# Kernel optimization log

Measured on AMD Instinct MI355X. Metric: run time of the kernel, lower is better.

The kernel has to match this reference:

```python
import jax, jax.numpy as jnp
import numpy as np

B, N = 32, 4096
SA1 = (512, 0.2, 32)   # npoint, radius, nsample
SA2 = (128, 0.4, 64)
MLP1 = [3, 64, 64, 128]
MLP2 = [131, 128, 128, 256]   # 128 feats + 3 relative xyz
MLP3 = [259, 256, 512, 1024]  # 256 feats + 3 xyz (group_all)


def _mk_mlp(key, dims, prefix, d):
    for i in range(len(dims) - 1):
        key, k1 = jax.random.split(key)
        d[f"{prefix}_w{i}"] = jax.random.normal(k1, (dims[i], dims[i + 1]), jnp.float32) * (1.0 / np.sqrt(dims[i]))
        d[f"{prefix}_b{i}"] = jnp.zeros((dims[i + 1],), jnp.float32)
    return key


def setup_inputs() -> dict:
    key = jax.random.key(0)
    d = {}
    key, kx = jax.random.split(key)
    d["xyz"] = jax.random.uniform(kx, (B, N, 3), jnp.float32)  # normalized coords in [0,1)
    key = _mk_mlp(key, MLP1, "sa1", d)
    key = _mk_mlp(key, MLP2, "sa2", d)
    key = _mk_mlp(key, MLP3, "sa3", d)
    key, k1, k2 = jax.random.split(key, 3)
    d["cls_w"] = jax.random.normal(k1, (1024, 1), jnp.float32) * 0.03
    d["cls_b"] = jnp.zeros((1,), jnp.float32)
    d["reg_w"] = jax.random.normal(k2, (1024, 4), jnp.float32) * 0.03
    d["reg_b"] = jnp.zeros((4,), jnp.float32)
    return d


def fps(xyz, npoint):
    """Farthest point sampling. xyz: (B,N,3) -> idx (B,npoint) int32."""
    Bb, Nn, _ = xyz.shape

    def step(carry, _):
        dist, farthest = carry  # (B,N), (B,)
        centroid = jnp.take_along_axis(xyz, farthest[:, None, None], axis=1)  # (B,1,3)
        d = jnp.sum((xyz - centroid) ** 2, axis=-1)  # (B,N)
        dist = jnp.minimum(dist, d)
        nxt = jnp.argmax(dist, axis=-1).astype(jnp.int32)
        return (dist, nxt), farthest

    init = (jnp.full((Bb, Nn), 1e10, xyz.dtype), jnp.zeros((Bb,), jnp.int32))
    _, idx = jax.lax.scan(step, init, None, length=npoint)
    return idx.T  # (B,npoint)


def ball_query(radius, nsample, xyz, new_xyz):
    """xyz: (B,N,3), new_xyz: (B,S,3) -> idx (B,S,nsample) int32."""
    Bb, S, _ = new_xyz.shape
    Nn = xyz.shape[1]
    sqr = jnp.sum((new_xyz[:, :, None, :] - xyz[:, None, :, :]) ** 2, axis=-1)  # (B,S,N)
    idx = jnp.broadcast_to(jnp.arange(Nn, dtype=jnp.int32), (Bb, S, Nn))
    idx = jnp.where(sqr > radius * radius, Nn, idx)
    idx = jnp.sort(idx, axis=-1)[:, :, :nsample]
    first = idx[:, :, :1]
    return jnp.where(idx == Nn, first, idx)  # pad out-of-ball slots with first neighbor


def _sa(xyz, feats, npoint, radius, nsample, ws, bs):
    Bb = xyz.shape[0]
    cidx = fps(xyz, npoint)
    new_xyz = xyz[jnp.arange(Bb)[:, None], cidx]  # (B,S,3)
    gidx = ball_query(radius, nsample, xyz, new_xyz)  # (B,S,K)
    b3 = jnp.arange(Bb)[:, None, None]
    g = xyz[b3, gidx] - new_xyz[:, :, None, :]  # (B,S,K,3) relative coords
    if feats is not None:
        g = jnp.concatenate([g, feats[b3, gidx]], axis=-1)
    for w, b in zip(ws, bs):
        g = jax.nn.relu(g @ w + b)
    return new_xyz, jnp.max(g, axis=2)  # (B,S,C_out)


def _sa_all(xyz, feats, ws, bs):
    g = jnp.concatenate([xyz, feats], axis=-1)[:, None]  # (B,1,S,3+C)
    for w, b in zip(ws, bs):
        g = jax.nn.relu(g @ w + b)
    return jnp.max(g, axis=2)[:, 0]  # (B,C_out)


def reference(xyz, sa1_w0, sa1_b0, sa1_w1, sa1_b1, sa1_w2, sa1_b2,
              sa2_w0, sa2_b0, sa2_w1, sa2_b1, sa2_w2, sa2_b2,
              sa3_w0, sa3_b0, sa3_w1, sa3_b1, sa3_w2, sa3_b2,
              cls_w, cls_b, reg_w, reg_b):
    xyz1, f1 = _sa(xyz, None, SA1[0], SA1[1], SA1[2],
                   [sa1_w0, sa1_w1, sa1_w2], [sa1_b0, sa1_b1, sa1_b2])
    xyz2, f2 = _sa(xyz1, f1, SA2[0], SA2[1], SA2[2],
                   [sa2_w0, sa2_w1, sa2_w2], [sa2_b0, sa2_b1, sa2_b2])
    feat = _sa_all(xyz2, f2, [sa3_w0, sa3_w1, sa3_w2], [sa3_b0, sa3_b1, sa3_b2])  # (B,1024)
    return feat @ cls_w + cls_b, feat @ reg_w + reg_b
```

## Files before the change

kernel.cpp:

```cpp
#include <hip/hip_runtime.h>
#include <hip/hip_bf16.h>

#define DEVINL __device__ __forceinline__

typedef __attribute__((ext_vector_type(8))) short bf16x8;
typedef __attribute__((ext_vector_type(8))) unsigned short u16x8;
typedef __attribute__((ext_vector_type(4))) float f32x4;

DEVINL unsigned short f2bh(float f){
  __hip_bfloat16 h = __float2bfloat16(f);
  return __bfloat16_as_ushort(h);
}
DEVINL float bh2f(unsigned short h){ return __uint_as_float(((unsigned)h) << 16); }

DEVINL unsigned long long dpp_max_u64(unsigned long long k) {
#define DPP_STEP(ctrl)                                                        \
  {                                                                           \
    int hi = (int)(k >> 32), lo = (int)(unsigned)k;                           \
    int oh = __builtin_amdgcn_update_dpp(0, hi, ctrl, 0xF, 0xF, 1);           \
    int ol = __builtin_amdgcn_update_dpp(0, lo, ctrl, 0xF, 0xF, 1);           \
    unsigned long long ok =                                                   \
        ((unsigned long long)(unsigned)oh << 32) | (unsigned)ol;              \
    if (ok > k) k = ok;                                                       \
  }
  DPP_STEP(0x111)
  DPP_STEP(0x112)
  DPP_STEP(0x114)
  DPP_STEP(0x118)
  DPP_STEP(0x142)
  DPP_STEP(0x143)
#undef DPP_STEP
  return k;
}

template<int N, int NP, int NT>
DEVINL void fps_body(const float* __restrict__ xyz, float* __restrict__ nxyz,
                     int b, int t) {
  constexpr int PTS = N / NT;
  constexpr int NW = NT / 64;
  __shared__ float xs[N], ys[N], zs[N];
  __shared__ int farr[NP];
  __shared__ unsigned long long sk[2][(NW > 1 ? NW : 1)];
  float px[PTS], py[PTS], pz[PTS], dst[PTS];
  const float* base = xyz + (size_t)b * N * 3;
#pragma unroll
  for (int j = 0; j < PTS; ++j) {
    int i = t + j * NT;
    float x = base[i * 3 + 0], y = base[i * 3 + 1], z = base[i * 3 + 2];
    px[j] = x; py[j] = y; pz[j] = z;
    xs[i] = x; ys[i] = y; zs[i] = z;
    dst[j] = 1e10f;
  }
  if constexpr (NW > 1) __syncthreads();
  int far = 0;
  const int wv = t >> 6, ln = t & 63;
  for (int s = 0; s < NP; ++s) {
    float cx = xs[far], cy = ys[far], cz = zs[far];
    if (t == 0) farr[s] = far;
    float bv = -1.f; int bi = 0;
#pragma unroll
    for (int j = 0; j < PTS; ++j) {
      float dx = __fsub_rn(px[j], cx), dy = __fsub_rn(py[j], cy), dz = __fsub_rn(pz[j], cz);
      float d = __fadd_rn(__fadd_rn(__fmul_rn(dx, dx), __fmul_rn(dy, dy)), __fmul_rn(dz, dz));
      float nd = fminf(dst[j], d);
      dst[j] = nd;
      int i = t + j * NT;
      if (nd > bv) { bv = nd; bi = i; }
    }
    unsigned long long key =
        ((unsigned long long)__float_as_uint(bv) << 32) | (unsigned)(~bi);
    key = dpp_max_u64(key);
    if constexpr (NW == 1) {
      int rl = __builtin_amdgcn_readlane((int)(unsigned)key, 63);
      far = (int)(~(unsigned)rl);
    } else {
      const int p = s & 1;
      if (ln == 63) sk[p][wv] = key;
      __syncthreads();
      unsigned long long m = sk[p][0];
#pragma unroll
      for (int q = 1; q < NW; ++q) {
        unsigned long long qk = sk[p][q];
        if (qk > m) m = qk;
      }
      far = (int)(~(unsigned)m);
    }
  }
  if constexpr (NW > 1) __syncthreads();
  for (int s2 = t; s2 < NP; s2 += NT) {
    int fi = farr[s2];
    float* o = nxyz + ((size_t)b * NP + s2) * 3;
    o[0] = xs[fi]; o[1] = ys[fi]; o[2] = zs[fi];
  }
}

template<int N, int NS>
DEVINL void bq_body(const float* __restrict__ pts, const float* __restrict__ centers,
                    int* __restrict__ gidx, int Q, float r2, int blk, int t) {
  const int wv = t >> 6, ln = t & 63;
  const int g = blk * 4 + wv;
  const int b = g / Q, q = g % Q;
  const float* pb = pts + (size_t)b * N * 3;
  const float* c = centers + ((size_t)b * Q + q) * 3;
  const float cx = c[0], cy = c[1], cz = c[2];
  __shared__ int gbuf[4][NS];
  float nx = pb[ln * 3 + 0], ny = pb[ln * 3 + 1], nz = pb[ln * 3 + 2];
  int taken = 0;
  for (int base = 0; base < N; base += 64) {
    const float x = nx, y = ny, z = nz;
    if (base + 64 < N) {
      const float* np = pb + (size_t)(base + 64 + ln) * 3;
      nx = np[0]; ny = np[1]; nz = np[2];
    }
    int i = base + ln;
    float dx = __fsub_rn(x, cx), dy = __fsub_rn(y, cy), dz = __fsub_rn(z, cz);
    float d = __fadd_rn(__fadd_rn(__fmul_rn(dx, dx), __fmul_rn(dy, dy)), __fmul_rn(dz, dz));
    bool in = (d <= r2);
    unsigned long long mk = __ballot(in);
    int rank = __popcll(mk & ((1ull << ln) - 1ull));
    int pos = taken + rank;
    if (in && pos < NS) gbuf[wv][pos] = i;
    taken += (int)__popcll(mk);
    if (taken >= NS) break;
  }
  int total = taken < NS ? taken : NS;
  int first = gbuf[wv][0];
  int* out = gidx + ((size_t)b * Q + q) * NS;
  for (int j = ln; j < NS; j += 64) out[j] = (j < total) ? gbuf[wv][j] : first;
}

struct WPEnt { const float* W; unsigned short* hi; unsigned short* lo; int K, N, row0, beg, end; };
struct WPTab { WPEnt e[8]; };
DEVINL void wprep_body(const WPTab& tab, int idx) {
#pragma unroll
  for (int i = 0; i < 8; ++i) {
    const WPEnt& E = tab.e[i];
    if (idx >= E.beg && idx < E.end) {
      int local = idx - E.beg;
      int k = local / E.N, n = local - k * E.N;
      float v = E.W[(size_t)(E.row0 + k) * E.N + n];
      unsigned short h = f2bh(v);
      E.hi[(size_t)n * E.K + k] = h;
      E.lo[(size_t)n * E.K + k] = f2bh(v - bh2f(h));
    }
  }
}

__global__ __launch_bounds__(256) void fps1_wprep_kernel(const float* __restrict__ xyz,
                                                         float* __restrict__ nx1, WPTab tab) {
  if (blockIdx.x < 32) { fps_body<4096, 512, 256>(xyz, nx1, blockIdx.x, threadIdx.x); return; }
  wprep_body(tab, (blockIdx.x - 32) * 256 + threadIdx.x);
}

__global__ __launch_bounds__(256) void fps2_bq1_kernel(const float* __restrict__ xyz,
                                                       const float* __restrict__ nx1,
                                                       int* __restrict__ gidx1,
                                                       float* __restrict__ nx2, float r21) {
  if (blockIdx.x < 32) {
    if (threadIdx.x < 64) fps_body<512, 128, 64>(nx1, nx2, blockIdx.x, threadIdx.x);
    return;
  }
  bq_body<4096, 32>(xyz, nx1, gidx1, 512, r21, blockIdx.x - 32, threadIdx.x);
}

template<int K, int N, int CW, int AS, int WS, bool XYZC, int NTH>
DEVINL void do_layer(const unsigned short* __restrict__ Ghi, const unsigned short* __restrict__ Glo,
                     const float* __restrict__ Wxyz,
                     const float* __restrict__ A, unsigned short* __restrict__ Whi,
                     unsigned short* __restrict__ Wlo, const float* __restrict__ sxyz,
                     f32x4* acc, int t) {
  constexpr int KT = K / 32;
  constexpr int NCH = N / CW;
  constexpr int K8 = K / 8;
  constexpr int SI = (CW * K8) / NTH;
  constexpr int CT = CW / 16;
  const int l = t & 63, wv = t >> 6;

  u16x8 rh[SI], rl[SI];
#pragma unroll
  for (int s = 0; s < SI; ++s) {
    int u = t + s * NTH;
    int nn = u / K8, k8 = (u - nn * K8) * 8;
    rh[s] = *reinterpret_cast<const u16x8*>(Ghi + (size_t)nn * K + k8);
    rl[s] = *reinterpret_cast<const u16x8*>(Glo + (size_t)nn * K + k8);
  }

  bf16x8 ahi[KT], alo[KT];
  {
    const int row = wv * 16 + (l & 15);
    const float* ap = A + row * AS + (l >> 4) * 8;
#pragma unroll
    for (int kt = 0; kt < KT; ++kt) {
      float4 v0 = *reinterpret_cast<const float4*>(ap + kt * 32);
      float4 v1 = *reinterpret_cast<const float4*>(ap + kt * 32 + 4);
      float f[8] = {v0.x, v0.y, v0.z, v0.w, v1.x, v1.y, v1.z, v1.w};
      bf16x8 h, lo2;
#pragma unroll
      for (int j = 0; j < 8; ++j) {
        unsigned short hb = f2bh(f[j]);
        h[j] = (short)hb;
        lo2[j] = (short)f2bh(f[j] - bh2f(hb));
      }
      ahi[kt] = h; alo[kt] = lo2;
    }
  }
#pragma unroll
  for (int i = 0; i < N / 16; ++i) acc[i] = f32x4{0.f, 0.f, 0.f, 0.f};

#pragma unroll
  for (int c = 0; c < NCH; ++c) {
    __syncthreads();
#pragma unroll
    for (int s = 0; s < SI; ++s) {
      int u = t + s * NTH;
      int nn = u / K8, k8 = (u - nn * K8) * 8;
      *reinterpret_cast<u16x8*>(Whi + nn * WS + k8) = rh[s];
      *reinterpret_cast<u16x8*>(Wlo + nn * WS + k8) = rl[s];
    }
    if (c + 1 < NCH) {
#pragma unroll
      for (int s = 0; s < SI; ++s) {
        int u = t + s * NTH;
        int nn = u / K8, k8 = (u - nn * K8) * 8;
        rh[s] = *reinterpret_cast<const u16x8*>(Ghi + (size_t)((c + 1) * CW + nn) * K + k8);
        rl[s] = *reinterpret_cast<const u16x8*>(Glo + (size_t)((c + 1) * CW + nn) * K + k8);
      }
    }
    __syncthreads();
#pragma unroll
    for (int ct = 0; ct < CT; ++ct) {
      const unsigned short* wp = Whi + (ct * 16 + (l & 15)) * WS + (l >> 4) * 8;
      const unsigned short* wq = Wlo + (ct * 16 + (l & 15)) * WS + (l >> 4) * 8;
      f32x4 a = acc[c * CT + ct];
#pragma unroll
      for (int kt = 0; kt < KT; ++kt) {
        bf16x8 wh = *reinterpret_cast<const bf16x8*>(wp + kt * 32);
        bf16x8 wl = *reinterpret_cast<const bf16x8*>(wq + kt * 32);
        a = __builtin_amdgcn_mfma_f32_16x16x32_bf16(ahi[kt], wh, a, 0, 0, 0);
        a = __builtin_amdgcn_mfma_f32_16x16x32_bf16(alo[kt], wh, a, 0, 0, 0);
        a = __builtin_amdgcn_mfma_f32_16x16x32_bf16(ahi[kt], wl, a, 0, 0, 0);
      }
      acc[c * CT + ct] = a;
    }
  }
  if constexpr (XYZC) {
    float xr[4][3];
#pragma unroll
    for (int r = 0; r < 4; ++r) {
      int row = wv * 16 + (l >> 4) * 4 + r;
      xr[r][0] = sxyz[row * 4 + 0];
      xr[r][1] = sxyz[row * 4 + 1];
      xr[r][2] = sxyz[row * 4 + 2];
    }
#pragma unroll
    for (int gt = 0; gt < N / 16; ++gt) {
      int col = gt * 16 + (l & 15);
      float w0 = Wxyz[col], w1 = Wxyz[N + col], w2 = Wxyz[2 * N + col];
#pragma unroll
      for (int r = 0; r < 4; ++r)
        acc[gt][r] += xr[r][0] * w0 + xr[r][1] * w1 + xr[r][2] * w2;
    }
  }
}

template<int NPTS, int Q, int M, int GPB, int FD, int C1, int C2, int C3>
__global__ __launch_bounds__(512) void sa2_kernel(
    const float* __restrict__ pts, const float* __restrict__ centers,
    const int* __restrict__ gidx, const float* __restrict__ feats,
    const float* __restrict__ W0, const float* __restrict__ B0,
    const unsigned short* __restrict__ G0h, const unsigned short* __restrict__ G0l,
    const unsigned short* __restrict__ G1h, const unsigned short* __restrict__ G1l,
    const float* __restrict__ B1,
    const unsigned short* __restrict__ G2h, const unsigned short* __restrict__ G2l,
    const float* __restrict__ B2,
    float* __restrict__ fout) {
  constexpr int NTH = 512;
  constexpr int ROWS = M * GPB;
  constexpr int NWV = NTH / 64;
  static_assert(ROWS == 16 * NWV, "wave owns 16 rows");
  constexpr int MK1 = (FD > C1 ? FD : C1);
  constexpr int MAXK = (MK1 > C2 ? MK1 : C2);
  constexpr int AS = MAXK + 12;
  constexpr int WS = MAXK + 8;
  constexpr int CW = 128;
  __shared__ __align__(16) float A[ROWS * AS];
  __shared__ __align__(16) unsigned short Whi[CW * WS];
  __shared__ __align__(16) unsigned short Wlo[CW * WS];
  __shared__ float sxyz[ROWS * 4];
  __shared__ int idxs[ROWS];
  __shared__ float ctr[GPB][4];
  __shared__ float red[NWV][C3];

  const int t = threadIdx.x;
  const int blk = blockIdx.x;
  const int b = blk / (Q / GPB);
  const int q0 = (blk % (Q / GPB)) * GPB;
  const int l = t & 63, wv = t >> 6;

  if (t < GPB * 3) {
    int g = t / 3, c2 = t % 3;
    ctr[g][c2] = centers[((size_t)b * Q + q0 + g) * 3 + c2];
  }
  for (int m = t; m < ROWS; m += NTH)
    idxs[m] = gidx[((size_t)b * Q + q0 + (m / M)) * M + (m % M)];
  __syncthreads();
  const float* pb = pts + (size_t)b * NPTS * 3;
  for (int u = t; u < ROWS * 3; u += NTH) {
    int m = u / 3, cmp = u - m * 3;
    int g = m / M, i = idxs[m];
    sxyz[m * 4 + cmp] = pb[i * 3 + cmp] - ctr[g][cmp];
  }
  {
    const int m = t >> 2, co = (t & 3) * (FD / 4);
    const float* src = feats + ((size_t)b * NPTS + idxs[m]) * FD + co;
    float* dst = A + m * AS + co;
#pragma unroll
    for (int j = 0; j < FD / 4; j += 4)
      *reinterpret_cast<float4*>(dst + j) = *reinterpret_cast<const float4*>(src + j);
  }
  __syncthreads();

  f32x4 acc[C3 / 16];

  do_layer<FD, C1, CW, AS, WS, true, NTH>(G0h, G0l, W0, A, Whi, Wlo, sxyz, acc, t);
#pragma unroll
  for (int gt = 0; gt < C1 / 16; ++gt) {
    int col = gt * 16 + (l & 15);
    float bia = B0[col];
#pragma unroll
    for (int r = 0; r < 4; ++r)
      A[(wv * 16 + (l >> 4) * 4 + r) * AS + col] = fmaxf(acc[gt][r] + bia, 0.f);
  }

  do_layer<C1, C2, CW, AS, WS, false, NTH>(G1h, G1l, nullptr, A, Whi, Wlo, sxyz, acc, t);
#pragma unroll
  for (int gt = 0; gt < C2 / 16; ++gt) {
    int col = gt * 16 + (l & 15);
    float bia = B1[col];
#pragma unroll
    for (int r = 0; r < 4; ++r)
      A[(wv * 16 + (l >> 4) * 4 + r) * AS + col] = fmaxf(acc[gt][r] + bia, 0.f);
  }

  do_layer<C2, C3, CW, AS, WS, false, NTH>(G2h, G2l, nullptr, A, Whi, Wlo, sxyz, acc, t);
#pragma unroll
  for (int gt = 0; gt < C3 / 16; ++gt) {
    int col = gt * 16 + (l & 15);
    float v = fmaxf(fmaxf(acc[gt][0], acc[gt][1]), fmaxf(acc[gt][2], acc[gt][3]));
    v = fmaxf(v, __shfl_xor(v, 16, 64));
    v = fmaxf(v, __shfl_xor(v, 32, 64));
    if (l < 16) red[wv][col] = v + B2[col];
  }
  __syncthreads();
  constexpr int WPG = NWV / GPB;
  for (int u = t; u < GPB * C3; u += NTH) {
    int g = u / C3, c2 = u - g * C3;
    float v = red[g * WPG][c2];
#pragma unroll
    for (int w = 1; w < WPG; ++w) v = fmaxf(v, red[g * WPG + w][c2]);
    fout[((size_t)b * Q + q0 + g) * C3 + c2] = fmaxf(v, 0.f);
  }
}

template<int NPTS, int Q, int M, int GPB, int TPB>
DEVINL void sa1_body(const float* __restrict__ pts, const float* __restrict__ centers,
                     const int* __restrict__ gidx,
                     const float* __restrict__ W0, const float* __restrict__ B0,
                     const unsigned short* __restrict__ G1h, const unsigned short* __restrict__ G1l,
                     const float* __restrict__ B1,
                     const unsigned short* __restrict__ G2h, const unsigned short* __restrict__ G2l,
                     const float* __restrict__ B2,
                     float* __restrict__ fout, int sblk, int t) {
  static_assert(M * GPB == 64, "");
  constexpr int C1 = 64, C2 = 64, C3 = 128;
  constexpr int AS = 76;
  constexpr int WS = 72;
  constexpr int NC = C2 + C3;
  __shared__ __align__(16) float A[64 * AS];
  __shared__ __align__(16) unsigned short Wh[NC * WS];
  __shared__ __align__(16) unsigned short Wl[NC * WS];
  __shared__ float sxyz[64 * 4];
  __shared__ int idxs[64];
  __shared__ float ctr[GPB][4];
  __shared__ float red[4][C3];

  const int l = t & 63, wv = t >> 6;

  for (int u = t; u < NC * 8; u += 256) {
    int col = u >> 3, k8 = (u & 7) * 8;
    const unsigned short* sh = (col < C2) ? G1h + (size_t)col * 64 + k8
                                          : G2h + (size_t)(col - C2) * 64 + k8;
    const unsigned short* sl = (col < C2) ? G1l + (size_t)col * 64 + k8
                                          : G2l + (size_t)(col - C2) * 64 + k8;
    *reinterpret_cast<u16x8*>(Wh + col * WS + k8) = *reinterpret_cast<const u16x8*>(sh);
    *reinterpret_cast<u16x8*>(Wl + col * WS + k8) = *reinterpret_cast<const u16x8*>(sl);
  }

  for (int it = 0; it < TPB; ++it) {
    const int blk = sblk * TPB + it;
    const int b = blk / (Q / GPB);
    const int q0 = (blk % (Q / GPB)) * GPB;

    if (t < GPB * 3) {
      int g = t / 3, c2 = t % 3;
      ctr[g][c2] = centers[((size_t)b * Q + q0 + g) * 3 + c2];
    }
    for (int m = t; m < 64; m += 256)
      idxs[m] = gidx[((size_t)b * Q + q0 + (m / M)) * M + (m % M)];
    __syncthreads();
    const float* pb = pts + (size_t)b * NPTS * 3;
    for (int u = t; u < 64 * 3; u += 256) {
      int m = u / 3, cmp = u - m * 3;
      int g = m / M, i = idxs[m];
      sxyz[m * 4 + cmp] = pb[i * 3 + cmp] - ctr[g][cmp];
    }
    __syncthreads();

    for (int u = t; u < 64 * C1; u += 256) {
      int m = u / C1, c2 = u - m * C1;
      float v = B0[c2] + sxyz[m * 4 + 0] * W0[0 * C1 + c2]
                       + sxyz[m * 4 + 1] * W0[1 * C1 + c2]
                       + sxyz[m * 4 + 2] * W0[2 * C1 + c2];
      A[m * AS + c2] = fmaxf(v, 0.f);
    }
    __syncthreads();

    f32x4 acc[8];
    {
      bf16x8 ah[2], al[2];
      const float* ap = A + (wv * 16 + (l & 15)) * AS + (l >> 4) * 8;
#pragma unroll
      for (int kt = 0; kt < 2; ++kt) {
        float4 v0 = *reinterpret_cast<const float4*>(ap + kt * 32);
        float4 v1 = *reinterpret_cast<const float4*>(ap + kt * 32 + 4);
        float f[8] = {v0.x, v0.y, v0.z, v0.w, v1.x, v1.y, v1.z, v1.w};
        bf16x8 h, lo2;
#pragma unroll
        for (int j = 0; j < 8; ++j) {
          unsigned short hb = f2bh(f[j]);
          h[j] = (short)hb;
          lo2[j] = (short)f2bh(f[j] - bh2f(hb));
        }
        ah[kt] = h; al[kt] = lo2;
      }
#pragma unroll
      for (int i = 0; i < 4; ++i) acc[i] = f32x4{0.f, 0.f, 0.f, 0.f};
#pragma unroll
      for (int ct = 0; ct < 4; ++ct) {
        const unsigned short* wp = Wh + (ct * 16 + (l & 15)) * WS + (l >> 4) * 8;
        const unsigned short* wq = Wl + (ct * 16 + (l & 15)) * WS + (l >> 4) * 8;
        f32x4 a = acc[ct];
#pragma unroll
        for (int kt = 0; kt < 2; ++kt) {
          bf16x8 wh = *reinterpret_cast<const bf16x8*>(wp + kt * 32);
          bf16x8 wl = *reinterpret_cast<const bf16x8*>(wq + kt * 32);
          a = __builtin_amdgcn_mfma_f32_16x16x32_bf16(ah[kt], wh, a, 0, 0, 0);
          a = __builtin_amdgcn_mfma_f32_16x16x32_bf16(al[kt], wh, a, 0, 0, 0);
          a = __builtin_amdgcn_mfma_f32_16x16x32_bf16(ah[kt], wl, a, 0, 0, 0);
        }
        acc[ct] = a;
      }
#pragma unroll
      for (int gt = 0; gt < 4; ++gt) {
        int col = gt * 16 + (l & 15);
        float bia = B1[col];
#pragma unroll
        for (int r = 0; r < 4; ++r)
          A[(wv * 16 + (l >> 4) * 4 + r) * AS + col] = fmaxf(acc[gt][r] + bia, 0.f);
      }
    }

    {
      bf16x8 ah[2], al[2];
      const float* ap = A + (wv * 16 + (l & 15)) * AS + (l >> 4) * 8;
#pragma unroll
      for (int kt = 0; kt < 2; ++kt) {
        float4 v0 = *reinterpret_cast<const float4*>(ap + kt * 32);
        float4 v1 = *reinterpret_cast<const float4*>(ap + kt * 32 + 4);
        float f[8] = {v0.x, v0.y, v0.z, v0.w, v1.x, v1.y, v1.z, v1.w};
        bf16x8 h, lo2;
#pragma unroll
        for (int j = 0; j < 8; ++j) {
          unsigned short hb = f2bh(f[j]);
          h[j] = (short)hb;
          lo2[j] = (short)f2bh(f[j] - bh2f(hb));
        }
        ah[kt] = h; al[kt] = lo2;
      }
#pragma unroll
      for (int i = 0; i < 8; ++i) acc[i] = f32x4{0.f, 0.f, 0.f, 0.f};
#pragma unroll
      for (int gt = 0; gt < 8; ++gt) {
        const unsigned short* wp = Wh + (C2 + gt * 16 + (l & 15)) * WS + (l >> 4) * 8;
        const unsigned short* wq = Wl + (C2 + gt * 16 + (l & 15)) * WS + (l >> 4) * 8;
        f32x4 a = acc[gt];
#pragma unroll
        for (int kt = 0; kt < 2; ++kt) {
          bf16x8 wh = *reinterpret_cast<const bf16x8*>(wp + kt * 32);
          bf16x8 wl = *reinterpret_cast<const bf16x8*>(wq + kt * 32);
          a = __builtin_amdgcn_mfma_f32_16x16x32_bf16(ah[kt], wh, a, 0, 0, 0);
          a = __builtin_amdgcn_mfma_f32_16x16x32_bf16(al[kt], wh, a, 0, 0, 0);
          a = __builtin_amdgcn_mfma_f32_16x16x32_bf16(ah[kt], wl, a, 0, 0, 0);
        }
        acc[gt] = a;
      }
#pragma unroll
      for (int gt = 0; gt < 8; ++gt) {
        int col = gt * 16 + (l & 15);
        float v = fmaxf(fmaxf(acc[gt][0], acc[gt][1]), fmaxf(acc[gt][2], acc[gt][3]));
        v = fmaxf(v, __shfl_xor(v, 16, 64));
        v = fmaxf(v, __shfl_xor(v, 32, 64));
        if (l < 16) red[wv][col] = v + B2[col];
      }
    }
    __syncthreads();
    constexpr int WPG = 4 / GPB;
    for (int u = t; u < GPB * C3; u += 256) {
      int g = u / C3, c2 = u - g * C3;
      float v = red[g * WPG][c2];
#pragma unroll
      for (int w = 1; w < WPG; ++w) v = fmaxf(v, red[g * WPG + w][c2]);
      fout[((size_t)b * Q + q0 + g) * C3 + c2] = fmaxf(v, 0.f);
    }
    __syncthreads();
  }
}

__global__ __launch_bounds__(256) void bq2_sa1_kernel(
    const float* __restrict__ xyz, const float* __restrict__ nx1,
    const float* __restrict__ nx2, int* __restrict__ gidx2, float r22,
    const int* __restrict__ gidx1,
    const float* __restrict__ s1w0, const float* __restrict__ s1b0,
    const unsigned short* __restrict__ g11h, const unsigned short* __restrict__ g11l,
    const float* __restrict__ s1b1,
    const unsigned short* __restrict__ g12h, const unsigned short* __restrict__ g12l,
    const float* __restrict__ s1b2, float* __restrict__ f1) {
  if (blockIdx.x < 1024) {
    bq_body<512, 64>(nx1, nx2, gidx2, 128, r22, blockIdx.x, threadIdx.x);
    return;
  }
  sa1_body<4096, 512, 32, 2, 8>(xyz, nx1, gidx1, s1w0, s1b0, g11h, g11l, s1b1,
                                g12h, g12l, s1b2, f1, blockIdx.x - 1024, threadIdx.x);
}

constexpr int AS3 = 532;
DEVINL void sa3_frags(const float* __restrict__ A, int l, int KT, bf16x8* ahi, bf16x8* alo) {
  const float* ap = A + (l & 15) * AS3 + (l >> 4) * 8;
  for (int kt = 0; kt < KT; ++kt) {
    float4 v0 = *reinterpret_cast<const float4*>(ap + kt * 32);
    float4 v1 = *reinterpret_cast<const float4*>(ap + kt * 32 + 4);
    float f[8] = {v0.x, v0.y, v0.z, v0.w, v1.x, v1.y, v1.z, v1.w};
    bf16x8 h, lo2;
#pragma unroll
    for (int j = 0; j < 8; ++j) {
      unsigned short hb = f2bh(f[j]);
      h[j] = (short)hb;
      lo2[j] = (short)f2bh(f[j] - bh2f(hb));
    }
    ahi[kt] = h; alo[kt] = lo2;
  }
}

template<int CT, int K>
DEVINL void sa3_mmN(const unsigned short* __restrict__ Gh, const unsigned short* __restrict__ Gl,
                    int ncol0, int l, const bf16x8* ahi, const bf16x8* alo, f32x4* acc4) {
  constexpr int KT = K / 32;
#pragma unroll
  for (int ct = 0; ct < CT; ++ct) {
    const unsigned short* hp = Gh + (size_t)(ncol0 + ct * 16 + (l & 15)) * K + (l >> 4) * 8;
    const unsigned short* lp = Gl + (size_t)(ncol0 + ct * 16 + (l & 15)) * K + (l >> 4) * 8;
    f32x4 a = acc4[ct];
#pragma unroll
    for (int kt = 0; kt < KT; ++kt) {
      bf16x8 wh = *reinterpret_cast<const bf16x8*>(hp + kt * 32);
      bf16x8 wl = *reinterpret_cast<const bf16x8*>(lp + kt * 32);
      a = __builtin_amdgcn_mfma_f32_16x16x32_bf16(ahi[kt], wh, a, 0, 0, 0);
      a = __builtin_amdgcn_mfma_f32_16x16x32_bf16(alo[kt], wh, a, 0, 0, 0);
      a = __builtin_amdgcn_mfma_f32_16x16x32_bf16(ahi[kt], wl, a, 0, 0, 0);
    }
    acc4[ct] = a;
  }
}

__global__ __launch_bounds__(512) void sa3f_kernel(
    const float* __restrict__ nx2, const float* __restrict__ f2,
    const float* __restrict__ W0full,
    const unsigned short* __restrict__ G0h, const unsigned short* __restrict__ G0l,
    const float* __restrict__ B0,
    const unsigned short* __restrict__ G1h, const unsigned short* __restrict__ G1l,
    const float* __restrict__ B1,
    const unsigned short* __restrict__ G2h, const unsigned short* __restrict__ G2l,
    const float* __restrict__ B2,
    float* __restrict__ partial) {
  __shared__ __align__(16) float A[16 * AS3];
  __shared__ float sxyz[16][4];
  const int t = threadIdx.x, l = t & 63, w = t >> 6;
  const int b = blockIdx.x >> 3, rb = blockIdx.x & 7;
  const int row0 = rb * 16;
  {
    int r = t >> 5, cc = (t & 31) * 8;
    const float* src = f2 + ((size_t)b * 128 + row0 + r) * 256 + cc;
    float* dstp = A + r * AS3 + cc;
#pragma unroll
    for (int j = 0; j < 8; j += 4)
      *reinterpret_cast<float4*>(dstp + j) = *reinterpret_cast<const float4*>(src + j);
    if (t < 16) {
      const float* s = nx2 + ((size_t)b * 128 + row0 + t) * 3;
      sxyz[t][0] = s[0]; sxyz[t][1] = s[1]; sxyz[t][2] = s[2];
    }
  }
  __syncthreads();

  {
    bf16x8 ah[8], al[8];
    sa3_frags(A, l, 8, ah, al);
    __syncthreads();
    f32x4 acc[2];
#pragma unroll
    for (int i = 0; i < 2; ++i) acc[i] = f32x4{0.f, 0.f, 0.f, 0.f};
    sa3_mmN<2, 256>(G0h, G0l, w * 32, l, ah, al, acc);
    float xr[4][3];
#pragma unroll
    for (int r = 0; r < 4; ++r) {
      int row = (l >> 4) * 4 + r;
      xr[r][0] = sxyz[row][0]; xr[r][1] = sxyz[row][1]; xr[r][2] = sxyz[row][2];
    }
#pragma unroll
    for (int ct = 0; ct < 2; ++ct) {
      int col = w * 32 + ct * 16 + (l & 15);
      float w0 = W0full[col], w1 = W0full[256 + col], w2 = W0full[512 + col];
      float bia = B0[col];
#pragma unroll
      for (int r = 0; r < 4; ++r) {
        int row = (l >> 4) * 4 + r;
        float v = acc[ct][r] + xr[r][0] * w0 + xr[r][1] * w1 + xr[r][2] * w2 + bia;
        A[row * AS3 + col] = fmaxf(v, 0.f);
      }
    }
    __syncthreads();
  }

  {
    bf16x8 ah[8], al[8];
    sa3_frags(A, l, 8, ah, al);
    __syncthreads();
    f32x4 acc[4];
#pragma unroll
    for (int i = 0; i < 4; ++i) acc[i] = f32x4{0.f, 0.f, 0.f, 0.f};
    sa3_mmN<4, 256>(G1h, G1l, w * 64, l, ah, al, acc);
#pragma unroll
    for (int cc = 0; cc < 4; ++cc) {
      int col = w * 64 + cc * 16 + (l & 15);
      float bia = B1[col];
#pragma unroll
      for (int r = 0; r < 4; ++r) {
        int row = (l >> 4) * 4 + r;
        A[row * AS3 + col] = fmaxf(acc[cc][r] + bia, 0.f);
      }
    }
    __syncthreads();
  }

  {
    bf16x8 ah[16], al[16];
    sa3_frags(A, l, 16, ah, al);
    float* pout = partial + ((size_t)(b * 8 + rb)) * 1024;
#pragma unroll
    for (int sub = 0; sub < 2; ++sub) {
      f32x4 acc[4];
#pragma unroll
      for (int i = 0; i < 4; ++i) acc[i] = f32x4{0.f, 0.f, 0.f, 0.f};
      sa3_mmN<4, 512>(G2h, G2l, w * 128 + sub * 64, l, ah, al, acc);
#pragma unroll
      for (int ct = 0; ct < 4; ++ct) {
        int col = w * 128 + sub * 64 + ct * 16 + (l & 15);
        float v = fmaxf(fmaxf(acc[ct][0], acc[ct][1]), fmaxf(acc[ct][2], acc[ct][3]));
        v = fmaxf(v, __shfl_xor(v, 16, 64));
        v = fmaxf(v, __shfl_xor(v, 32, 64));
        if (l < 16) pout[col] = v + B2[col];
      }
    }
  }
}

__global__ __launch_bounds__(256) void heads_kernel(const float* __restrict__ partial,
                                                    const float* __restrict__ cw,
                                                    const float* __restrict__ cb,
                                                    const float* __restrict__ rw,
                                                    const float* __restrict__ rb,
                                                    float* __restrict__ out) {
  const int b = blockIdx.x, t = threadIdx.x;
  const float* pb = partial + (size_t)b * 8 * 1024;
  float a0 = 0, a1 = 0, a2 = 0, a3 = 0, a4 = 0;
  for (int k = t; k < 1024; k += 256) {
    float m = pb[k];
#pragma unroll
    for (int p = 1; p < 8; ++p) m = fmaxf(m, pb[p * 1024 + k]);
    float f = fmaxf(m, 0.f);
    a0 += f * cw[k];
    const float* r = rw + (size_t)k * 4;
    a1 += f * r[0]; a2 += f * r[1]; a3 += f * r[2]; a4 += f * r[3];
  }
#pragma unroll
  for (int m = 32; m >= 1; m >>= 1) {
    a0 += __shfl_xor(a0, m, 64); a1 += __shfl_xor(a1, m, 64);
    a2 += __shfl_xor(a2, m, 64); a3 += __shfl_xor(a3, m, 64);
    a4 += __shfl_xor(a4, m, 64);
  }
  __shared__ float red[4][5];
  const int wv = t >> 6, ln = t & 63;
  if (ln == 0) { red[wv][0] = a0; red[wv][1] = a1; red[wv][2] = a2; red[wv][3] = a3; red[wv][4] = a4; }
  __syncthreads();
  if (t == 0) {
    float s0 = red[0][0] + red[1][0] + red[2][0] + red[3][0];
    float s1 = red[0][1] + red[1][1] + red[2][1] + red[3][1];
    float s2 = red[0][2] + red[1][2] + red[2][2] + red[3][2];
    float s3 = red[0][3] + red[1][3] + red[2][3] + red[3][3];
    float s4 = red[0][4] + red[1][4] + red[2][4] + red[3][4];
    out[b] = s0 + cb[0];
    out[32 + b * 4 + 0] = s1 + rb[0];
    out[32 + b * 4 + 1] = s2 + rb[1];
    out[32 + b * 4 + 2] = s3 + rb[2];
    out[32 + b * 4 + 3] = s4 + rb[3];
  }
}

extern "C" void kernel_launch(void* const* d_in, const int* in_sizes, int n_in,
                              void* d_out, int out_size, void* d_ws, size_t ws_size,
                              hipStream_t stream) {
  (void)in_sizes; (void)n_in; (void)out_size; (void)ws_size;
  const float* xyz  = (const float*)d_in[0];
  const float* s1w0 = (const float*)d_in[1];  const float* s1b0 = (const float*)d_in[2];
  const float* s1w1 = (const float*)d_in[3];  const float* s1b1 = (const float*)d_in[4];
  const float* s1w2 = (const float*)d_in[5];  const float* s1b2 = (const float*)d_in[6];
  const float* s2w0 = (const float*)d_in[7];  const float* s2b0 = (const float*)d_in[8];
  const float* s2w1 = (const float*)d_in[9];  const float* s2b1 = (const float*)d_in[10];
  const float* s2w2 = (const float*)d_in[11]; const float* s2b2 = (const float*)d_in[12];
  const float* s3w0 = (const float*)d_in[13]; const float* s3b0 = (const float*)d_in[14];
  const float* s3w1 = (const float*)d_in[15]; const float* s3b1 = (const float*)d_in[16];
  const float* s3w2 = (const float*)d_in[17]; const float* s3b2 = (const float*)d_in[18];
  const float* clsw = (const float*)d_in[19]; const float* clsb = (const float*)d_in[20];
  const float* regw = (const float*)d_in[21]; const float* regb = (const float*)d_in[22];

  char* ws = (char*)d_ws;
  float* nx1   = (float*)(ws + 0);
  int*   gidx1 = (int*)  (ws + 196608);
  float* f1    = (float*)(ws + 2293760);
  float* nx2   = (float*)(ws + 10682368);
  int*   gidx2 = (int*)  (ws + 10731520);
  float* f2    = (float*)(ws + 11780096);

  unsigned short* wt = (unsigned short*)(ws + 20168704);
  unsigned short* g11h = wt;
  unsigned short* g11l = wt + 4096;
  unsigned short* g12h = wt + 8192;
  unsigned short* g12l = wt + 16384;
  unsigned short* g20h = wt + 24576;
  unsigned short* g20l = wt + 40960;
  unsigned short* g21h = wt + 57344;
  unsigned short* g21l = wt + 73728;
  unsigned short* g22h = wt + 90112;
  unsigned short* g22l = wt + 122880;
  unsigned short* g30h = (unsigned short*)(ws + 20480000);
  unsigned short* g30l = (unsigned short*)(ws + 20611072);
  unsigned short* g31h = (unsigned short*)(ws + 20742144);
  unsigned short* g31l = (unsigned short*)(ws + 21004288);
  unsigned short* g32h = (unsigned short*)(ws + 21266432);
  unsigned short* g32l = (unsigned short*)(ws + 22315008);
  float* partial = (float*)(ws + 23363584);

  const float r21 = (float)(0.2 * 0.2);
  const float r22 = (float)(0.4 * 0.4);

  WPTab tab;
  int off = 0;
  auto set = [&](int i, const float* W, unsigned short* hi, unsigned short* lo,
                 int K, int N, int row0) {
    tab.e[i] = WPEnt{W, hi, lo, K, N, row0, off, off + K * N};
    off += K * N;
  };
  set(0, s1w1, g11h, g11l, 64, 64, 0);
  set(1, s1w2, g12h, g12l, 64, 128, 0);
  set(2, s2w0, g20h, g20l, 128, 128, 3);
  set(3, s2w1, g21h, g21l, 128, 128, 0);
  set(4, s2w2, g22h, g22l, 128, 256, 0);
  set(5, s3w0, g30h, g30l, 256, 256, 3);
  set(6, s3w1, g31h, g31l, 256, 512, 0);
  set(7, s3w2, g32h, g32l, 512, 1024, 0);
  const int wblocks = (off + 255) / 256;

  fps1_wprep_kernel<<<32 + wblocks, 256, 0, stream>>>(xyz, nx1, tab);
  fps2_bq1_kernel<<<32 + 4096, 256, 0, stream>>>(xyz, nx1, gidx1, nx2, r21);
  bq2_sa1_kernel<<<1024 + 1024, 256, 0, stream>>>(
      xyz, nx1, nx2, gidx2, r22, gidx1,
      s1w0, s1b0, g11h, g11l, s1b1, g12h, g12l, s1b2, f1);
  sa2_kernel<512, 128, 64, 2, 128, 128, 128, 256><<<2048, 512, 0, stream>>>(
      nx1, nx2, gidx2, f1, s2w0, s2b0,
      g20h, g20l, g21h, g21l, s2b1, g22h, g22l, s2b2, f2);
  sa3f_kernel<<<256, 512, 0, stream>>>(nx2, f2, s3w0, g30h, g30l, s3b0,
                                       g31h, g31l, s3b1, g32h, g32l, s3b2, partial);
  heads_kernel<<<32, 256, 0, stream>>>(partial, clsw, clsb, regw, regb, (float*)d_out);
}
```

Baseline: 643.9 us.

## Store SA1 features as split bf16 hi/lo and gather directly into SA2 MFMA operands

SA1 now writes its output features as pre-split bf16 high and low halves instead of fp32. SA2's first layer loads the gathered neighbour features straight from global memory into MFMA A-operand registers, skipping the fp32 LDS staging and the per-element hi/lo conversion. Gather traffic stays the same size, but the LDS round trip and conversion ALU work go away. The trade-off is uncoalesced 16-byte register gathers, plus the SA1 epilogue now has to do the split.

New measurement: 638.5 us (median of 2 runs). Within noise of the previous version (-0.8%).

```diff
diff --git a/kernel.cpp b/kernel.cpp
--- a/kernel.cpp
+++ b/kernel.cpp
@@ -163,12 +163,10 @@
   bq_body<4096, 32>(xyz, nx1, gidx1, 512, r21, blockIdx.x - 32, threadIdx.x);
 }
 
-template<int K, int N, int CW, int AS, int WS, bool XYZC, int NTH>
+template<int K, int N, int CW, int AS, int WS, int NTH>
 DEVINL void do_layer(const unsigned short* __restrict__ Ghi, const unsigned short* __restrict__ Glo,
-                     const float* __restrict__ Wxyz,
                      const float* __restrict__ A, unsigned short* __restrict__ Whi,
-                     unsigned short* __restrict__ Wlo, const float* __restrict__ sxyz,
-                     f32x4* acc, int t) {
+                     unsigned short* __restrict__ Wlo, f32x4* acc, int t) {
   constexpr int KT = K / 32;
   constexpr int NCH = N / CW;
   constexpr int K8 = K / 8;
@@ -243,7 +241,85 @@
       acc[c * CT + ct] = a;
     }
   }
-  if constexpr (XYZC) {
+}
+
+template<int K, int N, int CW, int WS, int NTH>
+DEVINL void do_layer0_gather(const unsigned short* __restrict__ Ghi,
+                             const unsigned short* __restrict__ Glo,
+                             const float* __restrict__ Wxyz,
+                             const unsigned short* __restrict__ f1h,
+                             const unsigned short* __restrict__ f1l,
+                             const int* __restrict__ idxs, const float* __restrict__ sxyz,
+                             unsigned short* __restrict__ Whi, unsigned short* __restrict__ Wlo,
+                             f32x4* acc, int t) {
+  constexpr int KT = K / 32;
+  constexpr int NCH = N / CW;
+  constexpr int K8 = K / 8;
+  constexpr int SI = (CW * K8) / NTH;
+  constexpr int CT = CW / 16;
+  const int l = t & 63, wv = t >> 6;
+
+  u16x8 rh[SI], rl[SI];
+#pragma unroll
+  for (int s = 0; s < SI; ++s) {
+    int u = t + s * NTH;
+    int nn = u / K8, k8 = (u - nn * K8) * 8;
+    rh[s] = *reinterpret_cast<const u16x8*>(Ghi + (size_t)nn * K + k8);
+    rl[s] = *reinterpret_cast<const u16x8*>(Glo + (size_t)nn * K + k8);
+  }
+
+  bf16x8 ahi[KT], alo[KT];
+  {
+    const int row = wv * 16 + (l & 15);
+    const int i = idxs[row];
+    const unsigned short* hp = f1h + (size_t)i * K + (l >> 4) * 8;
+    const unsigned short* lp = f1l + (size_t)i * K + (l >> 4) * 8;
+#pragma unroll
+    for (int kt = 0; kt < KT; ++kt) {
+      ahi[kt] = *reinterpret_cast<const bf16x8*>(hp + kt * 32);
+      alo[kt] = *reinterpret_cast<const bf16x8*>(lp + kt * 32);
+    }
+  }
+#pragma unroll
+  for (int i = 0; i < N / 16; ++i) acc[i] = f32x4{0.f, 0.f, 0.f, 0.f};
+
+#pragma unroll
+  for (int c = 0; c < NCH; ++c) {
+    __syncthreads();
+#pragma unroll
+    for (int s = 0; s < SI; ++s) {
+      int u = t + s * NTH;
+      int nn = u / K8, k8 = (u - nn * K8) * 8;
+      *reinterpret_cast<u16x8*>(Whi + nn * WS + k8) = rh[s];
+      *reinterpret_cast<u16x8*>(Wlo + nn * WS + k8) = rl[s];
+    }
+    if (c + 1 < NCH) {
+#pragma unroll
+      for (int s = 0; s < SI; ++s) {
+        int u = t + s * NTH;
+        int nn = u / K8, k8 = (u - nn * K8) * 8;
+        rh[s] = *reinterpret_cast<const u16x8*>(Ghi + (size_t)((c + 1) * CW + nn) * K + k8);
+        rl[s] = *reinterpret_cast<const u16x8*>(Glo + (size_t)((c + 1) * CW + nn) * K + k8);
+      }
+    }
+    __syncthreads();
+#pragma unroll
+    for (int ct = 0; ct < CT; ++ct) {
+      const unsigned short* wp = Whi + (ct * 16 + (l & 15)) * WS + (l >> 4) * 8;
+      const unsigned short* wq = Wlo + (ct * 16 + (l & 15)) * WS + (l >> 4) * 8;
+      f32x4 a = acc[c * CT + ct];
+#pragma unroll
+      for (int kt = 0; kt < KT; ++kt) {
+        bf16x8 wh = *reinterpret_cast<const bf16x8*>(wp + kt * 32);
+        bf16x8 wl = *reinterpret_cast<const bf16x8*>(wq + kt * 32);
+        a = __builtin_amdgcn_mfma_f32_16x16x32_bf16(ahi[kt], wh, a, 0, 0, 0);
+        a = __builtin_amdgcn_mfma_f32_16x16x32_bf16(alo[kt], wh, a, 0, 0, 0);
+        a = __builtin_amdgcn_mfma_f32_16x16x32_bf16(ahi[kt], wl, a, 0, 0, 0);
+      }
+      acc[c * CT + ct] = a;
+    }
+  }
+  {
     float xr[4][3];
 #pragma unroll
     for (int r = 0; r < 4; ++r) {
@@ -266,7 +342,8 @@
 template<int NPTS, int Q, int M, int GPB, int FD, int C1, int C2, int C3>
 __global__ __launch_bounds__(512) void sa2_kernel(
     const float* __restrict__ pts, const float* __restrict__ centers,
-    const int* __restrict__ gidx, const float* __restrict__ feats,
+    const int* __restrict__ gidx,
+    const unsigned short* __restrict__ f1h, const unsigned short* __restrict__ f1l,
     const float* __restrict__ W0, const float* __restrict__ B0,
     const unsigned short* __restrict__ G0h, const unsigned short* __restrict__ G0l,
     const unsigned short* __restrict__ G1h, const unsigned short* __restrict__ G1l,
@@ -278,8 +355,7 @@
   constexpr int ROWS = M * GPB;
   constexpr int NWV = NTH / 64;
   static_assert(ROWS == 16 * NWV, "wave owns 16 rows");
-  constexpr int MK1 = (FD > C1 ? FD : C1);
-  constexpr int MAXK = (MK1 > C2 ? MK1 : C2);
+  constexpr int MAXK = (C1 > C2 ? C1 : C2);
   constexpr int AS = MAXK + 12;
   constexpr int WS = MAXK + 8;
   constexpr int CW = 128;
@@ -310,19 +386,13 @@
     int g = m / M, i = idxs[m];
     sxyz[m * 4 + cmp] = pb[i * 3 + cmp] - ctr[g][cmp];
   }
-  {
-    const int m = t >> 2, co = (t & 3) * (FD / 4);
-    const float* src = feats + ((size_t)b * NPTS + idxs[m]) * FD + co;
-    float* dst = A + m * AS + co;
-#pragma unroll
-    for (int j = 0; j < FD / 4; j += 4)
-      *reinterpret_cast<float4*>(dst + j) = *reinterpret_cast<const float4*>(src + j);
-  }
   __syncthreads();
 
   f32x4 acc[C3 / 16];
 
-  do_layer<FD, C1, CW, AS, WS, true, NTH>(G0h, G0l, W0, A, Whi, Wlo, sxyz, acc, t);
+  do_layer0_gather<FD, C1, CW, WS, NTH>(
+      G0h, G0l, W0, f1h + (size_t)b * NPTS * FD, f1l + (size_t)b * NPTS * FD,
+      idxs, sxyz, Whi, Wlo, acc, t);
 #pragma unroll
   for (int gt = 0; gt < C1 / 16; ++gt) {
     int col = gt * 16 + (l & 15);
@@ -332,7 +402,7 @@
       A[(wv * 16 + (l >> 4) * 4 + r) * AS + col] = fmaxf(acc[gt][r] + bia, 0.f);
   }
 
-  do_layer<C1, C2, CW, AS, WS, false, NTH>(G1h, G1l, nullptr, A, Whi, Wlo, sxyz, acc, t);
+  do_layer<C1, C2, CW, AS, WS, NTH>(G1h, G1l, A, Whi, Wlo, acc, t);
 #pragma unroll
   for (int gt = 0; gt < C2 / 16; ++gt) {
     int col = gt * 16 + (l & 15);
@@ -342,7 +412,7 @@
       A[(wv * 16 + (l >> 4) * 4 + r) * AS + col] = fmaxf(acc[gt][r] + bia, 0.f);
   }
 
-  do_layer<C2, C3, CW, AS, WS, false, NTH>(G2h, G2l, nullptr, A, Whi, Wlo, sxyz, acc, t);
+  do_layer<C2, C3, CW, AS, WS, NTH>(G2h, G2l, A, Whi, Wlo, acc, t);
 #pragma unroll
   for (int gt = 0; gt < C3 / 16; ++gt) {
     int col = gt * 16 + (l & 15);
@@ -370,7 +440,8 @@
                      const float* __restrict__ B1,
                      const unsigned short* __restrict__ G2h, const unsigned short* __restrict__ G2l,
                      const float* __restrict__ B2,
-                     float* __restrict__ fout, int sblk, int t) {
+                     unsigned short* __restrict__ f1h, unsigned short* __restrict__ f1l,
+                     int sblk, int t) {
   static_assert(M * GPB == 64, "");
   constexpr int C1 = 64, C2 = 64, C3 = 128;
   constexpr int AS = 76;
@@ -520,7 +591,11 @@
       float v = red[g * WPG][c2];
 #pragma unroll
       for (int w = 1; w < WPG; ++w) v = fmaxf(v, red[g * WPG + w][c2]);
-      fout[((size_t)b * Q + q0 + g) * C3 + c2] = fmaxf(v, 0.f);
+      v = fmaxf(v, 0.f);
+      size_t o = ((size_t)b * Q + q0 + g) * C3 + c2;
+      unsigned short h = f2bh(v);
+      f1h[o] = h;
+      f1l[o] = f2bh(v - bh2f(h));
     }
     __syncthreads();
   }
@@ -534,13 +609,15 @@
     const unsigned short* __restrict__ g11h, const unsigned short* __restrict__ g11l,
     const float* __restrict__ s1b1,
     const unsigned short* __restrict__ g12h, const unsigned short* __restrict__ g12l,
-    const float* __restrict__ s1b2, float* __restrict__ f1) {
+    const float* __restrict__ s1b2,
+    unsigned short* __restrict__ f1h, unsigned short* __restrict__ f1l) {
   if (blockIdx.x < 1024) {
     bq_body<512, 64>(nx1, nx2, gidx2, 128, r22, blockIdx.x, threadIdx.x);
     return;
   }
   sa1_body<4096, 512, 32, 2, 8>(xyz, nx1, gidx1, s1w0, s1b0, g11h, g11l, s1b1,
-                                g12h, g12l, s1b2, f1, blockIdx.x - 1024, threadIdx.x);
+                                g12h, g12l, s1b2, f1h, f1l,
+                                blockIdx.x - 1024, threadIdx.x);
 }
 
 constexpr int AS3 = 532;
@@ -745,7 +822,8 @@
   char* ws = (char*)d_ws;
   float* nx1   = (float*)(ws + 0);
   int*   gidx1 = (int*)  (ws + 196608);
-  float* f1    = (float*)(ws + 2293760);
+  unsigned short* f1h = (unsigned short*)(ws + 2293760);
+  unsigned short* f1l = (unsigned short*)(ws + 6488064);
   float* nx2   = (float*)(ws + 10682368);
   int*   gidx2 = (int*)  (ws + 10731520);
   float* f2    = (float*)(ws + 11780096);
@@ -793,9 +871,9 @@
   fps2_bq1_kernel<<<32 + 4096, 256, 0, stream>>>(xyz, nx1, gidx1, nx2, r21);
   bq2_sa1_kernel<<<1024 + 1024, 256, 0, stream>>>(
       xyz, nx1, nx2, gidx2, r22, gidx1,
-      s1w0, s1b0, g11h, g11l, s1b1, g12h, g12l, s1b2, f1);
+      s1w0, s1b0, g11h, g11l, s1b1, g12h, g12l, s1b2, f1h, f1l);
   sa2_kernel<512, 128, 64, 2, 128, 128, 128, 256><<<2048, 512, 0, stream>>>(
-      nx1, nx2, gidx2, f1, s2w0, s2b0,
+      nx1, nx2, gidx2, f1h, f1l, s2w0, s2b0,
       g20h, g20l, g21h, g21l, s2b1, g22h, g22l, s2b2, f2);
   sa3f_kernel<<<256, 512, 0, stream>>>(nx2, f2, s3w0, g30h, g30l, s3b0,
                                        g31h, g31l, s3b1, g32h, g32l, s3b2, partial);
```
